# Optimization experiments

Hardware: AMD Instinct MI355X
Metric: run time of the kernel (lower is better)

## Reference

```python
import jax, jax.numpy as jnp
import numpy as np

EPS = 1e-12

def _layernorm(x, gamma, beta):
    m = jnp.mean(x, axis=-1, keepdims=True)
    v = jnp.mean((x - m) ** 2, axis=-1, keepdims=True)
    return (x - m) * jax.lax.rsqrt(v + EPS) * gamma + beta

def _gcn(x, node_emb, time_emb, W_pool, b_pool, gamma, beta):
    # x: [B, N, C]; node_emb: [N, D]; time_emb: [D]
    e = _layernorm(node_emb + time_emb[None, :], gamma, beta)          # [N, D] (dropout off: eval mode)
    A = jax.nn.softmax(e @ e.T, axis=1)                                 # [N, N] dynamic adjacency
    weights = jnp.einsum('nd,dkio->nkio', e, W_pool)                    # [N, 2, C, O] node-adaptive weights
    bias = e @ b_pool                                                   # [N, O]
    # supports = [I, A]; I support is identity -> x itself
    x_g = jnp.stack([x, jnp.einsum('nm,bmc->bnc', A, x)], axis=2)       # [B, N, 2, C]
    return jnp.einsum('bnki,nkio->bno', x_g, weights) + bias            # [B, N, O]

def setup_inputs() -> dict:
    key = jax.random.key(0)
    ks = jax.random.split(key, 16)
    B, N, Din, H, D = 64, 2048, 2, 64, 16
    C = Din + H
    inp = {
        'x': jax.random.normal(ks[0], (B, N, Din), jnp.float32),
        'state': jax.random.normal(ks[1], (B, N, H), jnp.float32),
        'node_embeddings': jax.random.normal(ks[2], (N, D), jnp.float32),
        'time_embeddings': jax.random.normal(ks[3], (D,), jnp.float32),
    }
    for i, g in enumerate(['z', 'r', 'u']):
        inp[f'W_{g}'] = jax.random.normal(ks[4 + 2 * i], (D, 2, C, H), jnp.float32) * 0.02
        inp[f'b_{g}'] = jax.random.normal(ks[5 + 2 * i], (D, H), jnp.float32) * 0.02
        inp[f'gamma_{g}'] = jnp.ones((D,), jnp.float32)
        inp[f'beta_{g}'] = jnp.zeros((D,), jnp.float32)
    return inp

def reference(x, state, node_embeddings, time_embeddings,
              W_z, b_z, gamma_z, beta_z,
              W_r, b_r, gamma_r, beta_r,
              W_u, b_u, gamma_u, beta_u):
    xs = jnp.concatenate([x, state], axis=-1)                           # [B, N, Din+H]
    z = jax.nn.sigmoid(_gcn(xs, node_embeddings, time_embeddings, W_z, b_z, gamma_z, beta_z))
    r = jax.nn.sigmoid(_gcn(xs, node_embeddings, time_embeddings, W_r, b_r, gamma_r, beta_r))
    cand = jnp.concatenate([x, z * state], axis=-1)
    hc = jnp.tanh(_gcn(cand, node_embeddings, time_embeddings, W_u, b_u, gamma_u, beta_u))
    return r * state + (1.0 - r) * hc
```

## Files before the change

### kernel.cpp

```cpp
#include <hip/hip_runtime.h>
#include <hip/hip_bf16.h>
#include <math.h>


typedef __attribute__((ext_vector_type(4))) float f4;
typedef __attribute__((ext_vector_type(8))) short s8;

#define B_   64
#define N_   2048
#define DIN  2
#define H_   64
#define D_   16
#define C_   66
#define KI   132
#define KIP  160
#define CB   4224

#define GLD16(gp, lp) __builtin_amdgcn_global_load_lds((const __attribute__((address_space(1))) void*)(gp), (__attribute__((address_space(3))) void*)(lp), 16, 0, 0)

static __device__ __forceinline__ ushort f2bf(float v) {
  __hip_bfloat16 h = __float2bfloat16(v);
  return *(ushort*)&h;
}
static __device__ __forceinline__ float bf2f(ushort u) {
  __hip_bfloat16 h = *(__hip_bfloat16*)&u;
  return __bfloat162float(h);
}
static __device__ __forceinline__ uint packbf(float a, float b) {
  return ((uint)f2bf(b) << 16) | f2bf(a);
}

__global__ void k_e(const float* __restrict__ node, const float* __restrict__ timee,
                    const float* __restrict__ g0, const float* __restrict__ b0,
                    const float* __restrict__ g1, const float* __restrict__ b1,
                    const float* __restrict__ g2, const float* __restrict__ b2,
                    float* __restrict__ e, ushort* __restrict__ ebf) {
  int n = blockIdx.x * blockDim.x + threadIdx.x;
  if (n >= N_) return;
  float v[D_]; float m = 0.f;
  #pragma unroll
  for (int d = 0; d < D_; ++d) { v[d] = node[n * D_ + d] + timee[d]; m += v[d]; }
  m *= (1.0f / D_);
  float var = 0.f;
  #pragma unroll
  for (int d = 0; d < D_; ++d) { float t = v[d] - m; var += t * t; }
  var *= (1.0f / D_);
  float r = rsqrtf(var + 1e-12f);
  float y[D_];
  #pragma unroll
  for (int d = 0; d < D_; ++d) y[d] = (v[d] - m) * r;
  const float* gs[3] = {g0, g1, g2};
  const float* bs[3] = {b0, b1, b2};
  #pragma unroll
  for (int g = 0; g < 3; ++g) {
    #pragma unroll
    for (int d = 0; d < D_; d += 2) {
      float o0 = y[d] * gs[g][d] + bs[g][d];
      float o1 = y[d + 1] * gs[g][d + 1] + bs[g][d + 1];
      e[g * N_ * D_ + n * D_ + d] = o0;
      e[g * N_ * D_ + n * D_ + d + 1] = o1;
      *(uint*)&ebf[g * N_ * D_ + n * D_ + d] = packbf(o0, o1);
    }
  }
}

__global__ __launch_bounds__(256)
void k_attn(const ushort* __restrict__ ebf, __hip_bfloat16* __restrict__ A) {
  __shared__ __align__(16) ushort eb[N_ * D_];
  __shared__ float red[4][16];
  const int t = threadIdx.x;
  const ushort* eg = ebf + (size_t)blockIdx.z * (N_ * D_);
  {
    const uint4* src = (const uint4*)eg;
    uint4* dst = (uint4*)eb;
    #pragma unroll
    for (int i = 0; i < 16; ++i) dst[i * 256 + t] = src[i * 256 + t];
  }
  __syncthreads();
  const int lane = t & 63, w = t >> 6;
  const int l15 = lane & 15, q = lane >> 4;
  const int r0 = blockIdx.x * 16;
  s8 af = {0, 0, 0, 0, 0, 0, 0, 0};
  if (q < 2) af = *(const s8*)&eb[(r0 + l15) * D_ + q * 8];
  const int c0 = w * 512;
  f4 acc[32];
  #pragma unroll
  for (int tl = 0; tl < 32; ++tl) {
    s8 bfr = {0, 0, 0, 0, 0, 0, 0, 0};
    if (q < 2) bfr = *(const s8*)&eb[(c0 + tl * 16 + l15) * D_ + q * 8];
    acc[tl] = __builtin_amdgcn_mfma_f32_16x16x32_bf16(af, bfr, (f4)0.0f, 0, 0, 0);
  }
  float pm[4], gm[4];
  #pragma unroll
  for (int rg = 0; rg < 4; ++rg) {
    float m = acc[0][rg];
    #pragma unroll
    for (int tl = 1; tl < 32; ++tl) m = fmaxf(m, acc[tl][rg]);
    m = fmaxf(m, __shfl_xor(m, 1, 64));
    m = fmaxf(m, __shfl_xor(m, 2, 64));
    m = fmaxf(m, __shfl_xor(m, 4, 64));
    m = fmaxf(m, __shfl_xor(m, 8, 64));
    pm[rg] = m;
  }
  if (l15 == 0) {
    #pragma unroll
    for (int rg = 0; rg < 4; ++rg) red[w][q * 4 + rg] = pm[rg];
  }
  __syncthreads();
  #pragma unroll
  for (int rg = 0; rg < 4; ++rg)
    gm[rg] = fmaxf(fmaxf(red[0][q * 4 + rg], red[1][q * 4 + rg]),
                   fmaxf(red[2][q * 4 + rg], red[3][q * 4 + rg]));
  __syncthreads();
  float ps[4] = {0.f, 0.f, 0.f, 0.f};
  #pragma unroll
  for (int tl = 0; tl < 32; ++tl) {
    #pragma unroll
    for (int rg = 0; rg < 4; ++rg) {
      float v = __expf(acc[tl][rg] - gm[rg]);
      acc[tl][rg] = v;
      ps[rg] += v;
    }
  }
  #pragma unroll
  for (int rg = 0; rg < 4; ++rg) {
    float s = ps[rg];
    s += __shfl_xor(s, 1, 64);
    s += __shfl_xor(s, 2, 64);
    s += __shfl_xor(s, 4, 64);
    s += __shfl_xor(s, 8, 64);
    if (l15 == 0) red[w][q * 4 + rg] = s;
  }
  __syncthreads();
  float inv[4];
  #pragma unroll
  for (int rg = 0; rg < 4; ++rg)
    inv[rg] = 1.0f / (red[0][q * 4 + rg] + red[1][q * 4 + rg] +
                      red[2][q * 4 + rg] + red[3][q * 4 + rg]);
  ushort* Ar = (ushort*)A + (size_t)blockIdx.z * ((size_t)N_ * N_);
  #pragma unroll
  for (int tl = 0; tl < 32; ++tl) {
    #pragma unroll
    for (int rg = 0; rg < 4; ++rg)
      Ar[(size_t)(r0 + q * 4 + rg) * N_ + c0 + tl * 16 + l15] = f2bf(acc[tl][rg] * inv[rg]);
  }
}

template <int MODE>
__global__ __launch_bounds__(256)
void k_buildX(const float* __restrict__ x, const float* __restrict__ state,
              const __hip_bfloat16* __restrict__ zbuf, __hip_bfloat16* __restrict__ XT) {
  constexpr int LDM = 72;
  __shared__ __align__(16) ushort T[C_ * LDM];
  const int t = threadIdx.x;
  const int m0 = blockIdx.x * 64, b = blockIdx.y;
  const int m = t >> 2, hq = t & 3;
  {
    const float* sp = state + ((size_t)b * N_ + m0 + m) * H_ + hq * 16;
    float sv[16];
    #pragma unroll
    for (int i = 0; i < 16; i += 4) {
      float4 v = *(const float4*)(sp + i);
      sv[i] = v.x; sv[i + 1] = v.y; sv[i + 2] = v.z; sv[i + 3] = v.w;
    }
    if (MODE) {
      const ushort* zp = (const ushort*)zbuf + ((size_t)b * N_ + m0 + m) * H_ + hq * 16;
      uint4 z0 = *(const uint4*)&zp[0], z1 = *(const uint4*)&zp[8];
      uint zw[8] = {z0.x, z0.y, z0.z, z0.w, z1.x, z1.y, z1.z, z1.w};
      #pragma unroll
      for (int i = 0; i < 8; ++i) {
        sv[2 * i]     *= bf2f((ushort)(zw[i] & 0xffffu));
        sv[2 * i + 1] *= bf2f((ushort)(zw[i] >> 16));
      }
    }
    #pragma unroll
    for (int i = 0; i < 16; ++i) T[(DIN + hq * 16 + i) * LDM + m] = f2bf(sv[i]);
    if (t < 64) {
      const float2 xv = *(const float2*)&x[((size_t)b * N_ + m0 + t) * DIN];
      T[0 * LDM + t] = f2bf(xv.x);
      T[1 * LDM + t] = f2bf(xv.y);
    }
  }
  __syncthreads();
  {
    int r = t >> 2, ch = t & 3;
    ushort* dst = (ushort*)XT + (size_t)(b * C_ + r) * N_ + m0 + ch * 16;
    *(uint4*)&dst[0] = *(uint4*)&T[r * LDM + ch * 16];
    *(uint4*)&dst[8] = *(uint4*)&T[r * LDM + ch * 16 + 8];
    if (t < 8) {
      r = 64 + (t >> 2);
      ushort* dst2 = (ushort*)XT + (size_t)(b * C_ + r) * N_ + m0 + ch * 16;
      *(uint4*)&dst2[0] = *(uint4*)&T[r * LDM + ch * 16];
      *(uint4*)&dst2[8] = *(uint4*)&T[r * LDM + ch * 16 + 8];
    }
  }
}

__global__ __launch_bounds__(256)
void k_gemm(const __hip_bfloat16* __restrict__ Abase, size_t astride,
            const __hip_bfloat16* __restrict__ XT,
            __hip_bfloat16* __restrict__ Ybase, size_t ystride) {
  __shared__ __align__(16) ushort At[2][128 * 32];
  __shared__ __align__(16) ushort Xt[2][128 * 32];
  const int t = threadIdx.x;
  const int nwg = gridDim.x * gridDim.y * gridDim.z;
  const int orig = blockIdx.x + gridDim.x * (blockIdx.y + gridDim.y * blockIdx.z);
  const int chunk = nwg >> 3;
  const int swz = (orig & 7) * chunk + (orig >> 3);
  const int bx = swz % gridDim.x;
  const int rest = swz / gridDim.x;
  const int by = rest % gridDim.y;
  const int bz = rest / gridDim.y;
  const int j0 = bx * 128, r0 = by * 128;
  const ushort* Ag = (const ushort*)Abase + (size_t)bz * astride;
  ushort* Y = (ushort*)Ybase + (size_t)bz * ystride;
  const int lane = t & 63, w = t >> 6;
  const int rowa = w * 32 + (lane >> 2), kc = (lane & 3) * 8;
  const ushort* gA = Ag + (size_t)(r0 + rowa) * N_ + kc;
  const ushort* gX = (const ushort*)XT + (size_t)(j0 + rowa) * N_ + kc;
  const int l15 = t & 15, q = (t >> 4) & 3;
  const int wr = (w >> 1) * 64, wc = (w & 1) * 64;
  f4 acc[4][4];
  #pragma unroll
  for (int i = 0; i < 4; ++i)
    #pragma unroll
    for (int jj = 0; jj < 4; ++jj) acc[i][jj] = (f4)0.0f;
  GLD16(gA, &At[0][(w * 32) * 32]);
  GLD16(gA + 16 * N_, &At[0][(w * 32 + 16) * 32]);
  GLD16(gX, &Xt[0][(w * 32) * 32]);
  GLD16(gX + 16 * N_, &Xt[0][(w * 32 + 16) * 32]);
  __syncthreads();
  int cur = 0;
  for (int k0 = 0; k0 < N_; k0 += 32) {
    const int kn = k0 + 32;
    if (kn < N_) {
      const int nx = cur ^ 1;
      GLD16(gA + kn, &At[nx][(w * 32) * 32]);
      GLD16(gA + 16 * N_ + kn, &At[nx][(w * 32 + 16) * 32]);
      GLD16(gX + kn, &Xt[nx][(w * 32) * 32]);
      GLD16(gX + 16 * N_ + kn, &Xt[nx][(w * 32 + 16) * 32]);
    }
    s8 af[4], bfr[4];
    #pragma unroll
    for (int mi = 0; mi < 4; ++mi) af[mi] = *(const s8*)&At[cur][(wr + mi * 16 + l15) * 32 + q * 8];
    #pragma unroll
    for (int ni = 0; ni < 4; ++ni) bfr[ni] = *(const s8*)&Xt[cur][(wc + ni * 16 + l15) * 32 + q * 8];
    #pragma unroll
    for (int mi = 0; mi < 4; ++mi)
      #pragma unroll
      for (int ni = 0; ni < 4; ++ni)
        acc[mi][ni] = __builtin_amdgcn_mfma_f32_16x16x32_bf16(af[mi], bfr[ni], acc[mi][ni], 0, 0, 0);
    __syncthreads();
    cur ^= 1;
  }
  #pragma unroll
  for (int mi = 0; mi < 4; ++mi) {
    int rr = r0 + wr + mi * 16 + q * 4;
    #pragma unroll
    for (int ni = 0; ni < 4; ++ni) {
      int cc = j0 + wc + ni * 16 + l15;
      #pragma unroll
      for (int rg = 0; rg < 4; ++rg)
        Y[(size_t)(rr + rg) * CB + cc] = f2bf(acc[mi][ni][rg]);
    }
  }
}

__global__ __launch_bounds__(256)
void k_wmat(const float* __restrict__ eg, const float* __restrict__ Wp, ushort* __restrict__ Wm) {
  constexpr int TRS = 36;
  __shared__ float Wl[16 * 8 * 64];
  __shared__ ushort Tr[8 * 64 * TRS];
  const int t = threadIdx.x;
  const int n0 = blockIdx.x * 8;
  const int y = blockIdx.y;
  const int o = t & 63, w = t >> 6;
  const int ng = w & 1, krh = (w >> 1) * 4;
  float er[4][16];
  #pragma unroll
  for (int j = 0; j < 4; ++j) {
    const float* ep = eg + (size_t)(n0 + ng * 4 + j) * D_;
    #pragma unroll
    for (int d = 0; d < D_; d += 4) {
      float4 v = *(const float4*)(ep + d);
      er[j][d] = v.x; er[j][d + 1] = v.y; er[j][d + 2] = v.z; er[j][d + 3] = v.w;
    }
  }
  const int ngroups = (y == 3) ? 2 : 1;
  for (int g = 0; g < ngroups; ++g) {
    const int kic0 = y * 4 + g * 4;
    for (int kk = 0; kk < 4; ++kk) {
      const int kic = kic0 + kk;
      __syncthreads();
      #pragma unroll
      for (int it = 0; it < 8; ++it) {
        int f = it * 256 + t;
        int d = f >> 7, rem = f & 127, kr = rem >> 4, o4 = rem & 15;
        int ki = kic * 8 + kr;
        float4 v;
        if (ki < KI) v = *(const float4*)&Wp[((size_t)d * KI + ki) * 64 + o4 * 4];
        else { v.x = 0.f; v.y = 0.f; v.z = 0.f; v.w = 0.f; }
        *(float4*)&Wl[f * 4] = v;
      }
      __syncthreads();
      float a[4][4];
      #pragma unroll
      for (int j = 0; j < 4; ++j)
        #pragma unroll
        for (int k = 0; k < 4; ++k) a[j][k] = 0.f;
      for (int d = 0; d < D_; ++d) {
        float w4[4];
        #pragma unroll
        for (int k = 0; k < 4; ++k) w4[k] = Wl[(d * 8 + krh + k) * 64 + o];
        #pragma unroll
        for (int j = 0; j < 4; ++j)
          #pragma unroll
          for (int k = 0; k < 4; ++k) a[j][k] = fmaf(er[j][d], w4[k], a[j][k]);
      }
      #pragma unroll
      for (int j = 0; j < 4; ++j) {
        ushort* tr = &Tr[((ng * 4 + j) * 64 + o) * TRS + kk * 8 + krh];
        *(uint*)&tr[0] = packbf(a[j][0], a[j][1]);
        *(uint*)&tr[2] = packbf(a[j][2], a[j][3]);
      }
    }
    __syncthreads();
    const int k0 = kic0 * 8;
    #pragma unroll
    for (int p = 0; p < 8; ++p) {
      int u = p * 256 + t;
      int nl = u >> 8, oo = (u >> 2) & 63, qq = u & 3;
      const ushort* tr = &Tr[(nl * 64 + oo) * TRS + qq * 8];
      uint2 lo = *(const uint2*)&tr[0];
      uint2 hi = *(const uint2*)&tr[4];
      uint4 vv; vv.x = lo.x; vv.y = lo.y; vv.z = hi.x; vv.w = hi.y;
      *(uint4*)&Wm[((size_t)(n0 + nl) * 64 + oo) * KIP + k0 + qq * 8] = vv;
    }
  }
}

template <int MODE>
__global__ __launch_bounds__(256)
void k_einsum(const float* __restrict__ e, const ushort* __restrict__ Wm, const float* __restrict__ bp,
              const __hip_bfloat16* __restrict__ Y,
              const float* __restrict__ x, const float* __restrict__ state,
              const __hip_bfloat16* __restrict__ zbuf, const __hip_bfloat16* __restrict__ rbuf,
              void* __restrict__ outp) {
  constexpr int LDK = 168;
  constexpr int LDR = 72;
  __shared__ __align__(16) ushort xg[64 * LDK];
  __shared__ __align__(16) ushort res[64 * LDR];
  __shared__ float el[D_];
  __shared__ float bl[64];
  const int n = blockIdx.x, t = threadIdx.x;
  if (t < D_) el[t] = e[n * D_ + t];
  __syncthreads();
  if (t < 64) {
    float s = 0.f;
    #pragma unroll
    for (int d = 0; d < D_; ++d) s += el[d] * bp[d * 64 + t];
    bl[t] = s;
  }
  {
    const int b = t >> 2, j = t & 3;
    const size_t bn = (size_t)b * N_ + n;
    float sv[16];
    const float* sp = state + bn * 64 + j * 16;
    #pragma unroll
    for (int i = 0; i < 16; i += 4) {
      float4 v = *(const float4*)(sp + i);
      sv[i] = v.x; sv[i + 1] = v.y; sv[i + 2] = v.z; sv[i + 3] = v.w;
    }
    if (MODE) {
      const ushort* zp = (const ushort*)zbuf + bn * 64 + j * 16;
      uint4 z0 = *(const uint4*)&zp[0], z1 = *(const uint4*)&zp[8];
      uint zw[8] = {z0.x, z0.y, z0.z, z0.w, z1.x, z1.y, z1.z, z1.w};
      #pragma unroll
      for (int i = 0; i < 8; ++i) {
        sv[2 * i]     *= bf2f((ushort)(zw[i] & 0xffffu));
        sv[2 * i + 1] *= bf2f((ushort)(zw[i] >> 16));
      }
    }
    ushort* xr = &xg[b * LDK + 2 + j * 16];
    #pragma unroll
    for (int i = 0; i < 16; i += 2) {
      uint pk = packbf(sv[i], sv[i + 1]);
      *(uint*)&xr[i] = pk;
    }
    const ushort* yp = (const ushort*)Y + (size_t)n * CB + b * C_ + j * 16;
    uint* xy = (uint*)&xg[b * LDK + 66 + j * 16];
    #pragma unroll
    for (int i = 0; i < 8; ++i) xy[i] = *(const uint*)&yp[2 * i];
    if (j == 0) *(uint*)&xg[b * LDK + 130] = *(const uint*)&yp[64];
    if (t < 64) {
      const float* xp = x + ((size_t)t * N_ + n) * DIN;
      uint pk = packbf(xp[0], xp[1]);
      *(uint*)&xg[t * LDK] = pk;
    }
    ushort* pg = &xg[b * LDK + 132 + j * 7];
    #pragma unroll
    for (int i = 0; i < 7; ++i) pg[i] = 0;
  }
  __syncthreads();
  const int l15 = t & 15, q = (t >> 4) & 3, w = t >> 6;
  const int wm = (w >> 1) * 32, wn = (w & 1) * 32;
  const ushort* Wn = Wm + (size_t)n * (64 * KIP);
  f4 acc[2][2];
  acc[0][0] = acc[0][1] = acc[1][0] = acc[1][1] = (f4)0.0f;
  #pragma unroll
  for (int kk = 0; kk < KIP; kk += 32) {
    s8 af[2], bfr[2];
    #pragma unroll
    for (int mi = 0; mi < 2; ++mi) af[mi] = *(const s8*)&xg[(wm + mi * 16 + l15) * LDK + kk + q * 8];
    #pragma unroll
    for (int ni = 0; ni < 2; ++ni) bfr[ni] = *(const s8*)(Wn + (size_t)(wn + ni * 16 + l15) * KIP + kk + q * 8);
    #pragma unroll
    for (int mi = 0; mi < 2; ++mi)
      #pragma unroll
      for (int ni = 0; ni < 2; ++ni)
        acc[mi][ni] = __builtin_amdgcn_mfma_f32_16x16x32_bf16(af[mi], bfr[ni], acc[mi][ni], 0, 0, 0);
  }
  {
    float bl0 = bl[wn + l15], bl1 = bl[wn + 16 + l15];
    #pragma unroll
    for (int mi = 0; mi < 2; ++mi)
      #pragma unroll
      for (int ni = 0; ni < 2; ++ni) {
        float bb = ni ? bl1 : bl0;
        #pragma unroll
        for (int rg = 0; rg < 4; ++rg) {
          float v = acc[mi][ni][rg] + bb;
          float a;
          if (MODE == 0) a = 1.0f / (1.0f + __expf(-v));
          else           a = 1.0f - 2.0f / (__expf(2.0f * v) + 1.0f);
          res[(wm + mi * 16 + q * 4 + rg) * LDR + (wn + ni * 16 + l15)] = f2bf(a);
        }
      }
  }
  __syncthreads();
  {
    const int b = t >> 2, j = t & 3;
    const size_t gb = ((size_t)b * N_ + n) * 64 + j * 16;
    const ushort* rr = &res[b * LDR + j * 16];
    if (MODE == 0) {
      uint4 v0 = *(const uint4*)&rr[0];
      uint4 v1 = *(const uint4*)&rr[8];
      *(uint4*)((ushort*)outp + gb) = v0;
      *(uint4*)((ushort*)outp + gb + 8) = v1;
    } else {
      float* ob = (float*)outp;
      const float* stp = state + gb;
      const ushort* rp = (const ushort*)rbuf + gb;
      uint4 r0 = *(const uint4*)&rp[0], r1 = *(const uint4*)&rp[8];
      uint rw[8] = {r0.x, r0.y, r0.z, r0.w, r1.x, r1.y, r1.z, r1.w};
      #pragma unroll
      for (int i = 0; i < 16; i += 4) {
        float4 st = *(const float4*)(stp + i);
        float4 ov;
        float rv0 = bf2f((ushort)(rw[i / 2] & 0xffffu));
        float rv1 = bf2f((ushort)(rw[i / 2] >> 16));
        float rv2 = bf2f((ushort)(rw[i / 2 + 1] & 0xffffu));
        float rv3 = bf2f((ushort)(rw[i / 2 + 1] >> 16));
        ov.x = rv0 * st.x + (1.0f - rv0) * bf2f(rr[i]);
        ov.y = rv1 * st.y + (1.0f - rv1) * bf2f(rr[i + 1]);
        ov.z = rv2 * st.z + (1.0f - rv2) * bf2f(rr[i + 2]);
        ov.w = rv3 * st.w + (1.0f - rv3) * bf2f(rr[i + 3]);
        *(float4*)(ob + gb + i) = ov;
      }
    }
  }
}

extern "C" void kernel_launch(void* const* d_in, const int* in_sizes, int n_in,
                              void* d_out, int out_size, void* d_ws, size_t ws_size,
                              hipStream_t stream) {
  const float* x     = (const float*)d_in[0];
  const float* state = (const float*)d_in[1];
  const float* node  = (const float*)d_in[2];
  const float* timee = (const float*)d_in[3];
  const float* W_z = (const float*)d_in[4];
  const float* b_z = (const float*)d_in[5];
  const float* g_z = (const float*)d_in[6];
  const float* be_z = (const float*)d_in[7];
  const float* W_r = (const float*)d_in[8];
  const float* b_r = (const float*)d_in[9];
  const float* g_r = (const float*)d_in[10];
  const float* be_r = (const float*)d_in[11];
  const float* W_u = (const float*)d_in[12];
  const float* b_u = (const float*)d_in[13];
  const float* g_u = (const float*)d_in[14];
  const float* be_u = (const float*)d_in[15];

  constexpr size_t NN = (size_t)N_ * N_;
  constexpr size_t ND = (size_t)N_ * D_;
  char* ws = (char*)d_ws;
  float*           e  = (float*)(ws);
  __hip_bfloat16*  A  = (__hip_bfloat16*)(ws + 393216);
  __hip_bfloat16*  XT = (__hip_bfloat16*)(ws + 25559040);
  __hip_bfloat16*  Y  = (__hip_bfloat16*)(ws + 42860544);
  __hip_bfloat16*  zb = (__hip_bfloat16*)(ws + 60162048);
  __hip_bfloat16*  rb = (__hip_bfloat16*)(ws + 76939264);
  ushort*          ebf = (ushort*)(ws + 93716480);
  ushort*          Wm = (ushort*)(ws + 93716480);
  __hip_bfloat16*  Yr = (__hip_bfloat16*)(ws + 135659520);
  const size_t YRD = ((size_t)135659520 - 42860544) / 2;
  const bool big = ws_size >= (size_t)152961024;

  float* out = (float*)d_out;

  k_e<<<8, 256, 0, stream>>>(node, timee, g_z, be_z, g_r, be_r, g_u, be_u, e, ebf);
  k_attn<<<dim3(N_ / 16, 1, 3), 256, 0, stream>>>(ebf, A);
  k_buildX<0><<<dim3(32, 64), 256, 0, stream>>>(x, state, nullptr, XT);

  dim3 ggrid1(CB / 128, N_ / 128, 1);
  dim3 ggrid2(CB / 128, N_ / 128, 2);
  dim3 wgrid(N_ / 8, 4);

  if (big) {
    k_wmat<<<wgrid, 256, 0, stream>>>(e + 0 * ND, W_z, Wm);
    k_gemm<<<ggrid2, 256, 0, stream>>>(A, NN, XT, Y, YRD);
    k_einsum<0><<<N_, 256, 0, stream>>>(e + 0 * ND, Wm, b_z, Y, x, state, nullptr, nullptr, (void*)zb);
    k_wmat<<<wgrid, 256, 0, stream>>>(e + 1 * ND, W_r, Wm);
    k_einsum<0><<<N_, 256, 0, stream>>>(e + 1 * ND, Wm, b_r, Yr, x, state, nullptr, nullptr, (void*)rb);
  } else {
    k_wmat<<<wgrid, 256, 0, stream>>>(e + 0 * ND, W_z, Wm);
    k_gemm<<<ggrid1, 256, 0, stream>>>(A, 0, XT, Y, 0);
    k_einsum<0><<<N_, 256, 0, stream>>>(e + 0 * ND, Wm, b_z, Y, x, state, nullptr, nullptr, (void*)zb);
    k_wmat<<<wgrid, 256, 0, stream>>>(e + 1 * ND, W_r, Wm);
    k_gemm<<<ggrid1, 256, 0, stream>>>(A + NN, 0, XT, Y, 0);
    k_einsum<0><<<N_, 256, 0, stream>>>(e + 1 * ND, Wm, b_r, Y, x, state, nullptr, nullptr, (void*)rb);
  }
  k_buildX<1><<<dim3(32, 64), 256, 0, stream>>>(x, state, zb, XT);
  k_wmat<<<wgrid, 256, 0, stream>>>(e + 2 * ND, W_u, Wm);
  k_gemm<<<ggrid1, 256, 0, stream>>>(A + 2 * NN, 0, XT, Y, 0);
  k_einsum<1><<<N_, 256, 0, stream>>>(e + 2 * ND, Wm, b_u, Y, x, state, zb, rb, (void*)out);
}
```

Measured before the change: 502.1 us.

## Swizzle GEMM LDS tiles, overlap loads with vmcnt waits, vectorize softmax stores

```diff
diff --git a/kernel.cpp b/kernel.cpp
--- a/kernel.cpp
+++ b/kernel.cpp
@@ -80,69 +80,51 @@
   const int lane = t & 63, w = t >> 6;
   const int l15 = lane & 15, q = lane >> 4;
   const int r0 = blockIdx.x * 16;
-  s8 af = {0, 0, 0, 0, 0, 0, 0, 0};
-  if (q < 2) af = *(const s8*)&eb[(r0 + l15) * D_ + q * 8];
+  s8 rf = {0, 0, 0, 0, 0, 0, 0, 0};
+  if (q < 2) rf = *(const s8*)&eb[(r0 + l15) * D_ + q * 8];
   const int c0 = w * 512;
   f4 acc[32];
   #pragma unroll
   for (int tl = 0; tl < 32; ++tl) {
-    s8 bfr = {0, 0, 0, 0, 0, 0, 0, 0};
-    if (q < 2) bfr = *(const s8*)&eb[(c0 + tl * 16 + l15) * D_ + q * 8];
-    acc[tl] = __builtin_amdgcn_mfma_f32_16x16x32_bf16(af, bfr, (f4)0.0f, 0, 0, 0);
-  }
-  float pm[4], gm[4];
-  #pragma unroll
-  for (int rg = 0; rg < 4; ++rg) {
-    float m = acc[0][rg];
-    #pragma unroll
-    for (int tl = 1; tl < 32; ++tl) m = fmaxf(m, acc[tl][rg]);
-    m = fmaxf(m, __shfl_xor(m, 1, 64));
-    m = fmaxf(m, __shfl_xor(m, 2, 64));
-    m = fmaxf(m, __shfl_xor(m, 4, 64));
-    m = fmaxf(m, __shfl_xor(m, 8, 64));
-    pm[rg] = m;
-  }
-  if (l15 == 0) {
-    #pragma unroll
-    for (int rg = 0; rg < 4; ++rg) red[w][q * 4 + rg] = pm[rg];
-  }
-  __syncthreads();
-  #pragma unroll
-  for (int rg = 0; rg < 4; ++rg)
-    gm[rg] = fmaxf(fmaxf(red[0][q * 4 + rg], red[1][q * 4 + rg]),
-                   fmaxf(red[2][q * 4 + rg], red[3][q * 4 + rg]));
-  __syncthreads();
-  float ps[4] = {0.f, 0.f, 0.f, 0.f};
+    s8 cf = {0, 0, 0, 0, 0, 0, 0, 0};
+    if (q < 2) cf = *(const s8*)&eb[(c0 + tl * 16 + l15) * D_ + q * 8];
+    acc[tl] = __builtin_amdgcn_mfma_f32_16x16x32_bf16(cf, rf, (f4)0.0f, 0, 0, 0);
+  }
+  float m = acc[0][0];
   #pragma unroll
   for (int tl = 0; tl < 32; ++tl) {
     #pragma unroll
+    for (int rg = 0; rg < 4; ++rg) m = fmaxf(m, acc[tl][rg]);
+  }
+  m = fmaxf(m, __shfl_xor(m, 16, 64));
+  m = fmaxf(m, __shfl_xor(m, 32, 64));
+  if (lane < 16) red[w][l15] = m;
+  __syncthreads();
+  const float gm = fmaxf(fmaxf(red[0][l15], red[1][l15]), fmaxf(red[2][l15], red[3][l15]));
+  __syncthreads();
+  float ps = 0.f;
+  #pragma unroll
+  for (int tl = 0; tl < 32; ++tl) {
+    #pragma unroll
     for (int rg = 0; rg < 4; ++rg) {
-      float v = __expf(acc[tl][rg] - gm[rg]);
+      float v = __expf(acc[tl][rg] - gm);
       acc[tl][rg] = v;
-      ps[rg] += v;
-    }
-  }
-  #pragma unroll
-  for (int rg = 0; rg < 4; ++rg) {
-    float s = ps[rg];
-    s += __shfl_xor(s, 1, 64);
-    s += __shfl_xor(s, 2, 64);
-    s += __shfl_xor(s, 4, 64);
-    s += __shfl_xor(s, 8, 64);
-    if (l15 == 0) red[w][q * 4 + rg] = s;
-  }
-  __syncthreads();
-  float inv[4];
-  #pragma unroll
-  for (int rg = 0; rg < 4; ++rg)
-    inv[rg] = 1.0f / (red[0][q * 4 + rg] + red[1][q * 4 + rg] +
-                      red[2][q * 4 + rg] + red[3][q * 4 + rg]);
-  ushort* Ar = (ushort*)A + (size_t)blockIdx.z * ((size_t)N_ * N_);
+      ps += v;
+    }
+  }
+  ps += __shfl_xor(ps, 16, 64);
+  ps += __shfl_xor(ps, 32, 64);
+  if (lane < 16) red[w][l15] = ps;
+  __syncthreads();
+  const float inv = 1.0f / (red[0][l15] + red[1][l15] + red[2][l15] + red[3][l15]);
+  ushort* Ar = (ushort*)A + (size_t)blockIdx.z * ((size_t)N_ * N_) +
+               (size_t)(r0 + l15) * N_ + c0 + q * 4;
   #pragma unroll
   for (int tl = 0; tl < 32; ++tl) {
-    #pragma unroll
-    for (int rg = 0; rg < 4; ++rg)
-      Ar[(size_t)(r0 + q * 4 + rg) * N_ + c0 + tl * 16 + l15] = f2bf(acc[tl][rg] * inv[rg]);
+    uint2 pk;
+    pk.x = packbf(acc[tl][0] * inv, acc[tl][1] * inv);
+    pk.y = packbf(acc[tl][2] * inv, acc[tl][3] * inv);
+    *(uint2*)&Ar[tl * 16] = pk;
   }
 }
 
@@ -215,42 +197,55 @@
   const ushort* Ag = (const ushort*)Abase + (size_t)bz * astride;
   ushort* Y = (ushort*)Ybase + (size_t)bz * ystride;
   const int lane = t & 63, w = t >> 6;
-  const int rowa = w * 32 + (lane >> 2), kc = (lane & 3) * 8;
-  const ushort* gA = Ag + (size_t)(r0 + rowa) * N_ + kc;
-  const ushort* gX = (const ushort*)XT + (size_t)(j0 + rowa) * N_ + kc;
+  const int rowa = w * 32 + (lane >> 2);
+  const int kc = (((lane & 3) ^ ((lane >> 3) & 3)) * 8);
+  const ushort* pA0 = Ag + (size_t)(r0 + rowa) * N_ + kc;
+  const ushort* pA1 = pA0 + 16 * N_;
+  const ushort* pX0 = (const ushort*)XT + (size_t)(j0 + rowa) * N_ + kc;
+  const ushort* pX1 = pX0 + 16 * N_;
   const int l15 = t & 15, q = (t >> 4) & 3;
+  const int qs = (q ^ ((l15 >> 1) & 3)) * 8;
   const int wr = (w >> 1) * 64, wc = (w & 1) * 64;
   f4 acc[4][4];
   #pragma unroll
   for (int i = 0; i < 4; ++i)
     #pragma unroll
     for (int jj = 0; jj < 4; ++jj) acc[i][jj] = (f4)0.0f;
-  GLD16(gA, &At[0][(w * 32) * 32]);
-  GLD16(gA + 16 * N_, &At[0][(w * 32 + 16) * 32]);
-  GLD16(gX, &Xt[0][(w * 32) * 32]);
-  GLD16(gX + 16 * N_, &Xt[0][(w * 32 + 16) * 32]);
-  __syncthreads();
+  GLD16(pA0, &At[0][(w * 32) * 32]);
+  GLD16(pA1, &At[0][(w * 32 + 16) * 32]);
+  GLD16(pX0, &Xt[0][(w * 32) * 32]);
+  GLD16(pX1, &Xt[0][(w * 32 + 16) * 32]);
+  pA0 += 32; pA1 += 32; pX0 += 32; pX1 += 32;
   int cur = 0;
   for (int k0 = 0; k0 < N_; k0 += 32) {
-    const int kn = k0 + 32;
-    if (kn < N_) {
+    if (k0 + 32 < N_) {
       const int nx = cur ^ 1;
-      GLD16(gA + kn, &At[nx][(w * 32) * 32]);
-      GLD16(gA + 16 * N_ + kn, &At[nx][(w * 32 + 16) * 32]);
-      GLD16(gX + kn, &Xt[nx][(w * 32) * 32]);
-      GLD16(gX + 16 * N_ + kn, &Xt[nx][(w * 32 + 16) * 32]);
-    }
+      GLD16(pA0, &At[nx][(w * 32) * 32]);
+      GLD16(pA1, &At[nx][(w * 32 + 16) * 32]);
+      GLD16(pX0, &Xt[nx][(w * 32) * 32]);
+      GLD16(pX1, &Xt[nx][(w * 32 + 16) * 32]);
+      pA0 += 32; pA1 += 32; pX0 += 32; pX1 += 32;
+      asm volatile("s_waitcnt vmcnt(4)" ::: "memory");
+    } else {
+      asm volatile("s_waitcnt vmcnt(0)" ::: "memory");
+    }
+    __builtin_amdgcn_s_barrier();
+    __builtin_amdgcn_sched_barrier(0);
     s8 af[4], bfr[4];
     #pragma unroll
-    for (int mi = 0; mi < 4; ++mi) af[mi] = *(const s8*)&At[cur][(wr + mi * 16 + l15) * 32 + q * 8];
-    #pragma unroll
-    for (int ni = 0; ni < 4; ++ni) bfr[ni] = *(const s8*)&Xt[cur][(wc + ni * 16 + l15) * 32 + q * 8];
+    for (int mi = 0; mi < 4; ++mi)
+      af[mi] = *(const s8*)&At[cur][(wr + mi * 16 + l15) * 32 + qs];
+    #pragma unroll
+    for (int ni = 0; ni < 4; ++ni)
+      bfr[ni] = *(const s8*)&Xt[cur][(wc + ni * 16 + l15) * 32 + qs];
+    __builtin_amdgcn_s_setprio(1);
     #pragma unroll
     for (int mi = 0; mi < 4; ++mi)
       #pragma unroll
       for (int ni = 0; ni < 4; ++ni)
         acc[mi][ni] = __builtin_amdgcn_mfma_f32_16x16x32_bf16(af[mi], bfr[ni], acc[mi][ni], 0, 0, 0);
-    __syncthreads();
+    __builtin_amdgcn_s_setprio(0);
+    __builtin_amdgcn_s_barrier();
     cur ^= 1;
   }
   #pragma unroll
```

After: 486.3 us. 3.2% less time.
